# Kernel tuning notes

Hardware: AMD Instinct MI355X
Metric: run time of the kernel (lower is better)

## Reference

```python
import jax, jax.numpy as jnp
import numpy as np

OUT, IN, GROUP = 4096, 4096, 128
NG = IN // GROUP  # 32 groups along in_features
TOKENS = 8192

def setup_inputs() -> dict:
    key = jax.random.key(0)
    k1, k2, k3, k4, k5 = jax.random.split(key, 5)
    input = jax.random.normal(k1, (TOKENS, IN), dtype=jnp.float32)
    qweight = jax.random.randint(k2, (OUT, IN), 0, 16, dtype=jnp.int32)
    scales = jax.random.uniform(k3, (OUT, NG), dtype=jnp.float32) * 0.02 + 0.001
    zeros = jax.random.uniform(k4, (OUT, NG), dtype=jnp.float32) * 15.0
    bias = jax.random.normal(k5, (OUT,), dtype=jnp.float32)
    return {"input": input, "qweight": qweight, "scales": scales, "zeros": zeros, "bias": bias}

def dequantize(qweight, scales, zeros):
    # qweight: [OUT, IN] int; scales/zeros: [OUT, NG]; group along in_features
    q = qweight.astype(jnp.float32).reshape(OUT, NG, GROUP)
    w = (q - zeros[:, :, None]) * scales[:, :, None]
    return w.reshape(OUT, IN)

def reference(input, qweight, scales, zeros, bias):
    # F.linear(input, W, bias) == input @ W.T + bias
    W = dequantize(qweight, scales, zeros)
    return jnp.einsum('ti,oi->to', input, W) + bias
```

## Files before the change

### kernel.cpp

```cpp
#include <hip/hip_runtime.h>
#include <hip/hip_bf16.h>
#include <cstdint>

typedef __attribute__((ext_vector_type(4))) float  floatx4;
typedef __attribute__((ext_vector_type(8))) __bf16 bf16x8;

#define M_T 8192
#define N_T 4096
#define K_T 4096
#define NG  32

__device__ __forceinline__ unsigned short f2bf(float f) {
    union { float f; unsigned int u; } v; v.f = f;
    unsigned int u = v.u;
    u += 0x7fffu + ((u >> 16) & 1u);
    return (unsigned short)(u >> 16);
}

__device__ __forceinline__ void load_lds16(const void* gsrc, void* ldst) {
    __builtin_amdgcn_global_load_lds(
        (const __attribute__((address_space(1))) uint32_t*)gsrc,
        (__attribute__((address_space(3))) uint32_t*)ldst,
        16, 0, 0);
}

__global__ void prep_kernel(const int* __restrict__ q,
                            const float* __restrict__ sc,
                            const float* __restrict__ zr,
                            const float* __restrict__ X,
                            unsigned short* __restrict__ Wb,
                            unsigned short* __restrict__ Xb) {
    int b = blockIdx.x;
    if (b < 16384) {
        int idx = b * 256 + threadIdx.x;
        int e0 = idx << 2;
        int row = e0 >> 12;
        int col = e0 & 4095;
        int g = col >> 7;
        float s = sc[(row << 5) + g];
        float z = zr[(row << 5) + g];
        int4 qv = *(const int4*)(q + e0);
        ushort4 o;
        o.x = f2bf(((float)qv.x - z) * s);
        o.y = f2bf(((float)qv.y - z) * s);
        o.z = f2bf(((float)qv.z - z) * s);
        o.w = f2bf(((float)qv.w - z) * s);
        *(ushort4*)(Wb + e0) = o;
    } else {
        int idx = (b - 16384) * 256 + threadIdx.x;
        int e0 = idx << 2;
        float4 xv = *(const float4*)(X + e0);
        ushort4 o;
        o.x = f2bf(xv.x); o.y = f2bf(xv.y); o.z = f2bf(xv.z); o.w = f2bf(xv.w);
        *(ushort4*)(Xb + e0) = o;
    }
}

__global__ __launch_bounds__(512, 2) void gemm256_8ph(
    const unsigned short* __restrict__ Xb,
    const unsigned short* __restrict__ Wb,
    const float* __restrict__ bias,
    float* __restrict__ C)
{
    __shared__ __align__(16) unsigned short lds[65536];
    char* ldsb = (char*)lds;

    const int tid  = threadIdx.x;
    const int lane = tid & 63;
    const int wid  = tid >> 6;
    const int wm   = wid >> 2;
    const int wn   = wid & 3;

    int bid = blockIdx.x;
    int xcd = bid & 7, r0 = bid >> 3;
    int mt = (xcd >> 1) * 8 + (r0 & 7);
    int nt = (xcd & 1) * 8 + (r0 >> 3);
    const int bm = mt * 256;
    const int bn = nt * 256;

    floatx4 acc[8][4] = {};

    const int klb  = (lane >> 4) * 16;
    const int axor = (lane & 7) << 4;

    int obA[2][2], obB[2][2];
    #pragma unroll
    for (int b = 0; b < 2; ++b)
        #pragma unroll
        for (int kp = 0; kp < 2; ++kp) {
            obA[b][kp] = b * 65536 + wm * 16384 + (lane & 15) * 128
                       + ((kp * 64 + klb) ^ axor);
            obB[b][kp] = b * 65536 + 32768 + (wn >> 1) * 16384 + (wn & 1) * 8192
                       + (lane & 15) * 128 + ((kp * 64 + klb) ^ axor);
        }

    auto rA = [&](int b, int kp, int mf) -> bf16x8 {
        return *(const bf16x8*)(ldsb + obA[b][kp] + mf * 2048);
    };
    auto rB = [&](int b, int kp, int nf) -> bf16x8 {
        return *(const bf16x8*)(ldsb + obB[b][kp] + nf * 2048);
    };

    const int pl0 = (wid * 8 + (lane >> 3)) * 8192
                  + (((lane & 7) * 16) ^ ((lane >> 3) << 4));
    const int pl1 = pl0 + 64 * 8192;
    const char* GA = (const char*)Xb + (size_t)bm * 8192;
    const char* GB = (const char*)Wb + (size_t)bn * 8192;

    auto stage_half = [&](int buf, int isB, int half, int tk, const char* G) {
        char* dst = ldsb + buf * 65536 + isB * 32768 + half * 16384 + wid * 1024;
        const char* s0 = G + ((size_t)half * 1048576 + (size_t)tk * 128);
        load_lds16(s0 + pl0, dst);
        load_lds16(s0 + pl1, dst + 8192);
    };

    stage_half(0, 1, 0, 0, GB);
    stage_half(0, 1, 1, 0, GB);
    stage_half(0, 0, 0, 0, GA);
    stage_half(0, 0, 1, 0, GA);
    stage_half(1, 1, 0, 1, GB);
    stage_half(1, 1, 1, 1, GB);
    asm volatile("s_waitcnt vmcnt(4)" ::: "memory");
    __builtin_amdgcn_s_barrier();
    asm volatile("" ::: "memory");

    bf16x8 a[4], bfr[4][2];
    #pragma unroll
    for (int nf = 0; nf < 4; ++nf) bfr[nf][0] = rB(0, 0, nf);
    #pragma unroll
    for (int m = 0; m < 4; ++m)    a[m] = rA(0, 0, m);

    for (int t = 0; t < 32; ++t) {
        const int t1 = 2 * t + 1;
        const int t2 = (2 * t + 2 < 64) ? 2 * t + 2 : 63;
        const int t3 = (2 * t + 3 < 64) ? 2 * t + 3 : 63;
        #pragma unroll
        for (int p = 0; p < 8; ++p) {
            const int cb    = p >> 2;
            const int q     = p & 3;
            const int kkp   = q >> 1;
            const int mbase = (q & 1) * 4;

            switch (p) {
                case 0: stage_half(1, 0, 0, t1, GA); break;
                case 1: stage_half(1, 0, 1, t1, GA); break;
                case 2: stage_half(0, 1, 0, t2, GB); break;
                case 3: stage_half(0, 1, 1, t2, GB); break;
                case 4: stage_half(0, 0, 0, t2, GA); break;
                case 5: stage_half(0, 0, 1, t2, GA); break;
                case 6: stage_half(1, 1, 0, t3, GB); break;
                case 7: stage_half(1, 1, 1, t3, GB); break;
            }

            __builtin_amdgcn_s_setprio(1);
            #pragma unroll
            for (int m = 0; m < 4; ++m)
                #pragma unroll
                for (int nf = 0; nf < 4; ++nf)
                    acc[mbase + m][nf] = __builtin_amdgcn_mfma_f32_16x16x32_bf16(
                        a[m], bfr[nf][kkp], acc[mbase + m][nf], 0, 0, 0);
            __builtin_amdgcn_s_setprio(0);

            if (q == 0) {
                #pragma unroll
                for (int nf = 0; nf < 4; ++nf) bfr[nf][1] = rB(cb, 1, nf);
                #pragma unroll
                for (int m = 0; m < 4; ++m)    a[m] = rA(cb, 0, 4 + m);
            } else if (q == 1) {
                #pragma unroll
                for (int m = 0; m < 4; ++m)    a[m] = rA(cb, 1, m);
            } else if (q == 2) {
                #pragma unroll
                for (int m = 0; m < 4; ++m)    a[m] = rA(cb, 1, 4 + m);
            } else {
                const int nb = cb ^ 1;
                #pragma unroll
                for (int nf = 0; nf < 4; ++nf) bfr[nf][0] = rB(nb, 0, nf);
                #pragma unroll
                for (int m = 0; m < 4; ++m)    a[m] = rA(nb, 0, m);
            }

            if (q == 1)
                asm volatile("s_waitcnt lgkmcnt(4)" ::: "memory");
            if (q == 2)
                asm volatile("s_waitcnt vmcnt(2)" ::: "memory");
            if (q != 0) {
                __builtin_amdgcn_s_barrier();
                asm volatile("" ::: "memory");
            }
        }
    }

    asm volatile("s_waitcnt vmcnt(0)" ::: "memory");

    #pragma unroll
    for (int nf = 0; nf < 4; ++nf) {
        int col = bn + wn * 64 + nf * 16 + (lane & 15);
        float bv = bias[col];
        #pragma unroll
        for (int mf = 0; mf < 8; ++mf) {
            int row0 = bm + wm * 128 + mf * 16 + (lane >> 4) * 4;
            #pragma unroll
            for (int j = 0; j < 4; ++j)
                C[(size_t)(row0 + j) * N_T + col] = acc[mf][nf][j] + bv;
        }
    }
}

__global__ void fallback_gemm(const float* __restrict__ X,
                              const int* __restrict__ q,
                              const float* __restrict__ sc,
                              const float* __restrict__ zr,
                              const float* __restrict__ bias,
                              float* __restrict__ C) {
    __shared__ float sX[16][17];
    __shared__ float sW[16][17];
    int tx = threadIdx.x, ty = threadIdx.y;
    int row = blockIdx.y * 16 + ty;
    int col = blockIdx.x * 16 + tx;
    float acc = 0.f;
    for (int k0 = 0; k0 < K_T; k0 += 16) {
        sX[ty][tx] = X[(size_t)row * K_T + k0 + tx];
        int wrow = blockIdx.x * 16 + ty;
        int kc = k0 + tx;
        int g = kc >> 7;
        sW[ty][tx] = ((float)q[(size_t)wrow * K_T + kc] - zr[wrow * NG + g]) * sc[wrow * NG + g];
        __syncthreads();
        #pragma unroll
        for (int kk = 0; kk < 16; ++kk) acc += sX[ty][kk] * sW[tx][kk];
        __syncthreads();
    }
    C[(size_t)row * N_T + col] = acc + bias[col];
}

extern "C" void kernel_launch(void* const* d_in, const int* in_sizes, int n_in,
                              void* d_out, int out_size, void* d_ws, size_t ws_size,
                              hipStream_t stream) {
    const float* input   = (const float*)d_in[0];
    const int*   qweight = (const int*)d_in[1];
    const float* scales  = (const float*)d_in[2];
    const float* zeros   = (const float*)d_in[3];
    const float* bias    = (const float*)d_in[4];
    float* out = (float*)d_out;

    const size_t needW = (size_t)N_T * K_T * sizeof(unsigned short);
    const size_t needX = (size_t)M_T * K_T * sizeof(unsigned short);

    if (ws_size >= needW + needX) {
        unsigned short* Wb = (unsigned short*)d_ws;
        unsigned short* Xb = (unsigned short*)((char*)d_ws + needW);

        prep_kernel<<<49152, 256, 0, stream>>>(qweight, scales, zeros, input, Wb, Xb);
        gemm256_8ph<<<512, 512, 0, stream>>>(Xb, Wb, bias, out);
    } else {
        dim3 blk(16, 16);
        dim3 grid(N_T / 16, M_T / 16);
        fallback_gemm<<<grid, blk, 0, stream>>>(input, qweight, scales, zeros, bias, out);
    }
}
```

Baseline: 275.7 us.

## Switch GEMM inner loop from 16x16x32 to 32x32x16 bf16 MFMA

```diff
diff --git a/kernel.cpp b/kernel.cpp
--- a/kernel.cpp
+++ b/kernel.cpp
@@ -2,8 +2,8 @@
 #include <hip/hip_bf16.h>
 #include <cstdint>
 
-typedef __attribute__((ext_vector_type(4))) float  floatx4;
-typedef __attribute__((ext_vector_type(8))) __bf16 bf16x8;
+typedef __attribute__((ext_vector_type(16))) float  floatx16;
+typedef __attribute__((ext_vector_type(8)))  __bf16 bf16x8;
 
 #define M_T 8192
 #define N_T 4096
@@ -56,7 +56,7 @@
     }
 }
 
-__global__ __launch_bounds__(512, 2) void gemm256_8ph(
+__global__ __launch_bounds__(512, 2) void gemm256_32x32(
     const unsigned short* __restrict__ Xb,
     const unsigned short* __restrict__ Wb,
     const float* __restrict__ bias,
@@ -78,27 +78,28 @@
     const int bm = mt * 256;
     const int bn = nt * 256;
 
-    floatx4 acc[8][4] = {};
-
-    const int klb  = (lane >> 4) * 16;
-    const int axor = (lane & 7) << 4;
-
-    int obA[2][2], obB[2][2];
+    floatx16 acc[4][2] = {};
+
+    const int l31  = lane & 31;
+    const int ksub = (lane >> 5) * 16;
+    const int xorv = (lane & 7) << 4;
+
+    int obA[2][4], obB[2][4];
     #pragma unroll
     for (int b = 0; b < 2; ++b)
         #pragma unroll
-        for (int kp = 0; kp < 2; ++kp) {
-            obA[b][kp] = b * 65536 + wm * 16384 + (lane & 15) * 128
-                       + ((kp * 64 + klb) ^ axor);
-            obB[b][kp] = b * 65536 + 32768 + (wn >> 1) * 16384 + (wn & 1) * 8192
-                       + (lane & 15) * 128 + ((kp * 64 + klb) ^ axor);
+        for (int k = 0; k < 4; ++k) {
+            obA[b][k] = b * 65536 + wm * 16384 + l31 * 128
+                      + ((k * 32 + ksub) ^ xorv);
+            obB[b][k] = b * 65536 + 32768 + (wn >> 1) * 16384 + (wn & 1) * 8192
+                      + l31 * 128 + ((k * 32 + ksub) ^ xorv);
         }
 
-    auto rA = [&](int b, int kp, int mf) -> bf16x8 {
-        return *(const bf16x8*)(ldsb + obA[b][kp] + mf * 2048);
+    auto rA = [&](int b, int k, int mf) -> bf16x8 {
+        return *(const bf16x8*)(ldsb + obA[b][k] + mf * 4096);
     };
-    auto rB = [&](int b, int kp, int nf) -> bf16x8 {
-        return *(const bf16x8*)(ldsb + obB[b][kp] + nf * 2048);
+    auto rB = [&](int b, int k, int nf) -> bf16x8 {
+        return *(const bf16x8*)(ldsb + obB[b][k] + nf * 4096);
     };
 
     const int pl0 = (wid * 8 + (lane >> 3)) * 8192
@@ -126,9 +127,11 @@
 
     bf16x8 a[4], bfr[4][2];
     #pragma unroll
-    for (int nf = 0; nf < 4; ++nf) bfr[nf][0] = rB(0, 0, nf);
-    #pragma unroll
-    for (int m = 0; m < 4; ++m)    a[m] = rA(0, 0, m);
+    for (int k = 0; k < 4; ++k)
+        #pragma unroll
+        for (int nf = 0; nf < 2; ++nf) bfr[k][nf] = rB(0, k, nf);
+    #pragma unroll
+    for (int m = 0; m < 4; ++m) a[m] = rA(0, 0, m);
 
     for (int t = 0; t < 32; ++t) {
         const int t1 = 2 * t + 1;
@@ -136,10 +139,8 @@
         const int t3 = (2 * t + 3 < 64) ? 2 * t + 3 : 63;
         #pragma unroll
         for (int p = 0; p < 8; ++p) {
-            const int cb    = p >> 2;
-            const int q     = p & 3;
-            const int kkp   = q >> 1;
-            const int mbase = (q & 1) * 4;
+            const int cb = p >> 2;
+            const int q  = p & 3;
 
             switch (p) {
                 case 0: stage_half(1, 0, 0, t1, GA); break;
@@ -156,26 +157,30 @@
             #pragma unroll
             for (int m = 0; m < 4; ++m)
                 #pragma unroll
-                for (int nf = 0; nf < 4; ++nf)
-                    acc[mbase + m][nf] = __builtin_amdgcn_mfma_f32_16x16x32_bf16(
-                        a[m], bfr[nf][kkp], acc[mbase + m][nf], 0, 0, 0);
+                for (int nf = 0; nf < 2; ++nf)
+                    acc[m][nf] = __builtin_amdgcn_mfma_f32_32x32x16_bf16(
+                        a[m], bfr[q][nf], acc[m][nf], 0, 0, 0);
             __builtin_amdgcn_s_setprio(0);
 
             if (q == 0) {
                 #pragma unroll
-                for (int nf = 0; nf < 4; ++nf) bfr[nf][1] = rB(cb, 1, nf);
-                #pragma unroll
-                for (int m = 0; m < 4; ++m)    a[m] = rA(cb, 0, 4 + m);
+                for (int nf = 0; nf < 2; ++nf) bfr[2][nf] = rB(cb, 2, nf);
+                #pragma unroll
+                for (int nf = 0; nf < 2; ++nf) bfr[3][nf] = rB(cb, 3, nf);
+                #pragma unroll
+                for (int m = 0; m < 4; ++m)    a[m] = rA(cb, 1, m);
             } else if (q == 1) {
                 #pragma unroll
-                for (int m = 0; m < 4; ++m)    a[m] = rA(cb, 1, m);
+                for (int m = 0; m < 4; ++m)    a[m] = rA(cb, 2, m);
             } else if (q == 2) {
                 #pragma unroll
-                for (int m = 0; m < 4; ++m)    a[m] = rA(cb, 1, 4 + m);
+                for (int m = 0; m < 4; ++m)    a[m] = rA(cb, 3, m);
             } else {
                 const int nb = cb ^ 1;
                 #pragma unroll
-                for (int nf = 0; nf < 4; ++nf) bfr[nf][0] = rB(nb, 0, nf);
+                for (int nf = 0; nf < 2; ++nf) bfr[0][nf] = rB(nb, 0, nf);
+                #pragma unroll
+                for (int nf = 0; nf < 2; ++nf) bfr[1][nf] = rB(nb, 1, nf);
                 #pragma unroll
                 for (int m = 0; m < 4; ++m)    a[m] = rA(nb, 0, m);
             }
@@ -194,15 +199,17 @@
     asm volatile("s_waitcnt vmcnt(0)" ::: "memory");
 
     #pragma unroll
-    for (int nf = 0; nf < 4; ++nf) {
-        int col = bn + wn * 64 + nf * 16 + (lane & 15);
+    for (int nf = 0; nf < 2; ++nf) {
+        int col = bn + wn * 64 + nf * 32 + l31;
         float bv = bias[col];
         #pragma unroll
-        for (int mf = 0; mf < 8; ++mf) {
-            int row0 = bm + wm * 128 + mf * 16 + (lane >> 4) * 4;
+        for (int mf = 0; mf < 4; ++mf) {
+            int rbase = bm + wm * 128 + mf * 32 + 4 * (lane >> 5);
             #pragma unroll
-            for (int j = 0; j < 4; ++j)
-                C[(size_t)(row0 + j) * N_T + col] = acc[mf][nf][j] + bv;
+            for (int r = 0; r < 16; ++r) {
+                int row = rbase + (r & 3) + 8 * (r >> 2);
+                C[(size_t)row * N_T + col] = acc[mf][nf][r] + bv;
+            }
         }
     }
 }
@@ -251,7 +258,7 @@
         unsigned short* Xb = (unsigned short*)((char*)d_ws + needW);
 
         prep_kernel<<<49152, 256, 0, stream>>>(qweight, scales, zeros, input, Wb, Xb);
-        gemm256_8ph<<<512, 512, 0, stream>>>(Xb, Wb, bias, out);
+        gemm256_32x32<<<512, 512, 0, stream>>>(Xb, Wb, bias, out);
     } else {
         dim3 blk(16, 16);
         dim3 grid(N_T / 16, M_T / 16);
```

After: 288.7 us. 1.05x slower.
